# Kernel tuning notes

Measured on AMD Instinct MI355X. Metric: run time of the kernel, lower is better.

The kernel has to match this reference:

```python
import jax, jax.numpy as jnp
import numpy as np

HID = 128
GRID = 8
PRED_LEN = 25


def _lstm_final(x, w_ih, w_hh, b_ih, b_hh):
    """PyTorch-style LSTM over time axis; returns final (h, c). x: [B, T, F]."""
    B = x.shape[0]
    H = w_hh.shape[1]
    # precompute input contribution for all timesteps: [B, T, 4H]
    gx = jnp.einsum('btf,gf->btg', x, w_ih) + b_ih + b_hh

    def step(carry, g):
        h, c = carry
        gates = g + h @ w_hh.T
        i, f, gg, o = jnp.split(gates, 4, axis=-1)  # torch gate order i,f,g,o
        i = jax.nn.sigmoid(i)
        f = jax.nn.sigmoid(f)
        gg = jnp.tanh(gg)
        o = jax.nn.sigmoid(o)
        c = f * c + i * gg
        h = o * jnp.tanh(c)
        return (h, c), None

    h0 = jnp.zeros((B, H), x.dtype)
    (h, c), _ = jax.lax.scan(step, (h0, h0), jnp.swapaxes(gx, 0, 1))
    return h, c


def _conv2d_same(x, w, b):
    y = jax.lax.conv_general_dilated(x, w, (1, 1), 'SAME',
                                     dimension_numbers=('NCHW', 'OIHW', 'NCHW'))
    return y + b[None, :, None, None]


def setup_inputs() -> dict:
    key = jax.random.key(0)
    ks = jax.random.split(key, 24)
    B, K, T, F = 8192, 8, 20, 7
    H = HID
    s = lambda fan: 1.0 / np.sqrt(fan)
    u = lambda k, shape, fan: jax.random.uniform(k, shape, jnp.float32, -s(fan), s(fan))
    inp = {
        'target': jax.random.normal(ks[0], (B, T, F), jnp.float32),
        'neigh_dyn': jax.random.normal(ks[1], (B, K, T, F), jnp.float32),
        'neigh_spatial': jax.random.normal(ks[2], (B, K, 2), jnp.float32),
        'lane': jax.random.normal(ks[3], (B, T), jnp.float32),
        # encoder LSTM
        'enc_w_ih': u(ks[4], (4 * H, F), H), 'enc_w_hh': u(ks[5], (4 * H, H), H),
        'enc_b_ih': u(ks[6], (4 * H,), H), 'enc_b_hh': u(ks[7], (4 * H,), H),
        # neighbor encoder LSTM
        'nb_w_ih': u(ks[8], (4 * H, F), H), 'nb_w_hh': u(ks[9], (4 * H, H), H),
        'nb_b_ih': u(ks[10], (4 * H,), H), 'nb_b_hh': u(ks[11], (4 * H,), H),
        # social conv stack
        'conv1_w': u(ks[12], (H // 2, H, 3, 3), H * 9), 'conv1_b': u(ks[13], (H // 2,), H * 9),
        'conv2_w': u(ks[14], (H // 4, H // 2, 3, 3), (H // 2) * 9), 'conv2_b': u(ks[15], (H // 4,), (H // 2) * 9),
        # fusion linear (H + H//4 -> H)
        'fus_w': u(ks[16], (H, H + H // 4), H + H // 4), 'fus_b': u(ks[17], (H,), H + H // 4),
        # decoder LSTM (input_dim 2)
        'dec_w_ih': u(ks[18], (4 * H, 2), H), 'dec_w_hh': u(ks[19], (4 * H, H), H),
        'dec_b_ih': u(ks[20], (4 * H,), H), 'dec_b_hh': u(ks[21], (4 * H,), H),
        # output linear (H -> 2)
        'out_w': u(ks[22], (2, H), H), 'out_b': u(ks[23], (2,), H),
    }
    return inp


def reference(target, neigh_dyn, neigh_spatial, lane,
              enc_w_ih, enc_w_hh, enc_b_ih, enc_b_hh,
              nb_w_ih, nb_w_hh, nb_b_ih, nb_b_hh,
              conv1_w, conv1_b, conv2_w, conv2_b,
              fus_w, fus_b,
              dec_w_ih, dec_w_hh, dec_b_ih, dec_b_hh,
              out_w, out_b):
    B = target.shape[0]
    K = neigh_dyn.shape[1]
    H = HID

    # encode target trajectory
    h_target, _ = _lstm_final(target, enc_w_ih, enc_w_hh, enc_b_ih, enc_b_hh)  # [B, H]

    # encode neighbors (shared weights) via flattening B*K
    neigh_flat = neigh_dyn.reshape(B * K, neigh_dyn.shape[2], neigh_dyn.shape[3])
    h_neigh, _ = _lstm_final(neigh_flat, nb_w_ih, nb_w_hh, nb_b_ih, nb_b_hh)
    h_neigh = h_neigh.reshape(B, K, H)

    # social pooling: scatter into [B, H, GRID, GRID]
    center = GRID // 2
    n = min(K, GRID * GRID - 1)
    idx = np.arange(n) + 1
    xs = idx % GRID
    ys = idx // GRID
    grid = jnp.zeros((B, H, GRID, GRID), target.dtype)
    grid = grid.at[:, :, center, center].set(h_target)
    grid = grid.at[:, :, ys, xs].set(jnp.swapaxes(h_neigh[:, :n, :], 1, 2))

    x = jax.nn.relu(_conv2d_same(grid, conv1_w, conv1_b))
    x = jax.nn.relu(_conv2d_same(x, conv2_w, conv2_b))
    pooled = jnp.max(x, axis=(2, 3))  # AdaptiveMaxPool2d(1) -> [B, H//4]

    fused = jnp.tanh(jnp.concatenate([h_target, pooled], axis=-1) @ fus_w.T + fus_b)

    dec_bias = dec_b_ih + dec_b_hh

    def dec_step(carry, _):
        h, c, inp = carry
        gates = inp @ dec_w_ih.T + h @ dec_w_hh.T + dec_bias
        i, f, gg, o = jnp.split(gates, 4, axis=-1)
        i = jax.nn.sigmoid(i)
        f = jax.nn.sigmoid(f)
        gg = jnp.tanh(gg)
        o = jax.nn.sigmoid(o)
        c = f * c + i * gg
        h = o * jnp.tanh(c)
        pred = h @ out_w.T + out_b  # [B, 2]
        return (h, c, pred), pred

    h0 = fused
    c0 = jnp.zeros_like(fused)
    inp0 = jnp.zeros((B, 2), target.dtype)
    _, preds = jax.lax.scan(dec_step, (h0, c0, inp0), None, length=PRED_LEN)
    return jnp.swapaxes(preds, 0, 1)  # [B, pred_len, 2]
```

## Files before the change

kernel.cpp:

```cpp
#include <hip/hip_runtime.h>

typedef _Float16 half8  __attribute__((ext_vector_type(8)));
typedef _Float16 half4v __attribute__((ext_vector_type(4)));
typedef float  floatx4  __attribute__((ext_vector_type(4)));

#define MFMA16(A,B,C) __builtin_amdgcn_mfma_f32_16x16x32_f16((A),(B),(C),0,0,0)

#define L2E  1.4426950408889634f
#define L2E2 2.8853900817779268f

__device__ __forceinline__ float rcpf(float x){ return __builtin_amdgcn_rcpf(x); }
__device__ __forceinline__ float ex2(float x){ return __builtin_amdgcn_exp2f(x); }
__device__ __forceinline__ float tanh_raw(float c){
  return 1.0f - 2.0f*rcpf(1.0f + ex2(L2E2*c));
}
__device__ __forceinline__ half8 ld8(const _Float16* p){
  half4v a = *(const half4v*)p;
  half4v b = *(const half4v*)(p+4);
  return __builtin_shufflevector(a,b,0,1,2,3,4,5,6,7);
}

__device__ __forceinline__ float lstm_cell(float yi, float yf, float yg, float yo,
                                           float& c){
  float A = ex2(-yi), B = ex2(-yf), C = ex2(yg);
  float r1 = rcpf(1.0f + B);
  float r2 = rcpf((1.0f + A)*(1.0f + C));
  float cn = c*r1 + (C - 1.0f)*r2;
  c = cn;
  float F = ex2(-yo), E = ex2(L2E2*cn);
  float r3 = rcpf((1.0f + F)*(1.0f + E));
  return (E - 1.0f)*r3;
}

static __device__ constexpr int DY[27] = {0,0,0,0,0,0,0,0, 1,1,1,1,1,1,1,1, 2,2, 3,3,3,4,4,4,5,5,5};
static __device__ constexpr int DX[27] = {0,1,2,3,4,5,6,7, 0,1,2,3,4,5,6,7, 0,1, 3,4,5,3,4,5,3,4,5};
static __device__ constexpr int PY[9]  = {0,0,0,0,0,0,0,1,4};
static __device__ constexpr int PX[9]  = {1,2,3,4,5,6,7,0,4};
static __device__ constexpr int OY[46] = {0,0,0,0,0,0,0,0, 1,1,1,1,1,1,1,1, 2,2,2,2,2,2,2,2,
                                          3,3,3,3,3,3,3, 4,4,4,4,4, 5,5,5,5,5, 6,6,6,6,6};
static __device__ constexpr int OX[46] = {0,1,2,3,4,5,6,7, 0,1,2,3,4,5,6,7, 0,1,2,3,4,5,6,7,
                                          0,1,2,3,4,5,6, 2,3,4,5,6, 2,3,4,5,6, 2,3,4,5,6};
__device__ constexpr int d1idx(int iy,int ix){
  return (iy<0||iy>7||ix<0||ix>7) ? -1 :
         (iy<=1) ? iy*8+ix :
         (iy==2 && ix<=1) ? 16+ix :
         (iy>=3 && iy<=5 && ix>=3 && ix<=5) ? 18+(iy-3)*3+(ix-3) : -1;
}

__global__ __launch_bounds__(512, 4) void lstm_all(
    const float* __restrict__ target, const float* __restrict__ neigh,
    const float* __restrict__ e_wih, const float* __restrict__ e_whh,
    const float* __restrict__ e_bih, const float* __restrict__ e_bhh,
    const float* __restrict__ n_wih, const float* __restrict__ n_whh,
    const float* __restrict__ n_bih, const float* __restrict__ n_bhh,
    _Float16* __restrict__ h_enc16, _Float16* __restrict__ h_nb16)
{
  __shared__ _Float16 h_lds[2][16][136];
  __shared__ _Float16 xf16[16][168];
  __shared__ __align__(16) _Float16 wihb[8][4][17][8];

  const int tid  = threadIdx.x;
  const int wv   = tid >> 6;
  const int lane = tid & 63;
  const int q    = lane >> 4;
  const int cb   = lane & 15;

  const bool enc = (blockIdx.x < 512);
  const float* x   = enc ? target : neigh;
  const float* wih = enc ? e_wih : n_wih;
  const float* whh = enc ? e_whh : n_whh;
  const float* bih = enc ? e_bih : n_bih;
  const float* bhh = enc ? e_bhh : n_bhh;
  _Float16* hout   = enc ? h_enc16 : h_nb16;
  const long base  = enc ? (long)blockIdx.x*16 : (long)(blockIdx.x-512)*16;

  for (int i = tid; i < 16*168; i += 512){
    int seq = i/168, rem = i%168, t = rem>>3, f = rem&7;
    float v = 0.f;
    if (t < 20) v = (f < 7) ? x[base*140 + seq*140 + t*7 + f] : 1.0f;
    xf16[seq][rem] = (_Float16)v;
  }
  for (int i = tid; i < 2*16*136; i += 512) ((_Float16*)h_lds)[i] = (_Float16)0.f;

  if (q == 0){
    #pragma unroll
    for (int g=0; g<4; ++g){
      const float sc = (g==2) ? L2E2 : L2E;
      const int col = g*128 + wv*16 + cb;
      _Float16* d = &wihb[wv][g][cb][0];
      #pragma unroll
      for (int j=0;j<7;++j) d[j] = (_Float16)(wih[col*7+j]*sc);
      d[7] = (_Float16)((bih[col]+bhh[col])*sc);
    }
  } else if (lane == 16){
    #pragma unroll
    for (int g=0; g<4; ++g){
      _Float16* d = &wihb[wv][g][16][0];
      #pragma unroll
      for (int j=0;j<8;++j) d[j] = (_Float16)0.f;
    }
  }

  half8 bfrag[4][4];
  #pragma unroll
  for (int g=0; g<4; ++g){
    const float sc = (g==2) ? L2E2 : L2E;
    const int col = g*128 + wv*16 + cb;
    #pragma unroll
    for (int kc=0; kc<4; ++kc){
      const float* src = whh + (long)col*128 + kc*32 + q*8;
      half8 f;
      #pragma unroll
      for (int j=0;j<8;++j) f[j] = (_Float16)(src[j]*sc);
      bfrag[g][kc] = f;
    }
  }
  __syncthreads();

  const _Float16* bxp = &wihb[wv][0][(q==0)?cb:16][0];
  const _Float16* a4p = (q==0) ? &xf16[cb][0] : &wihb[wv][0][16][0];
  const int a4step = (q==0) ? 8 : 0;
  half8 a4 = *(const half8*)a4p;
  a4p += a4step;

  float c_reg[4] = {0,0,0,0};
  half4v hv = {0,0,0,0};
  const floatx4 ZERO4 = {0.f,0.f,0.f,0.f};

  for (int t=0; t<20; ++t){
    const _Float16* hrow = &h_lds[t&1][cb][0];

    floatx4 acc[4];
    #pragma unroll
    for (int g=0; g<4; ++g){
      half8 bx = *(const half8*)(bxp + g*136);
      acc[g] = MFMA16(bx, a4, ZERO4);
    }
    #pragma unroll
    for (int kc=0; kc<4; ++kc){
      half8 b = *(const half8*)(hrow + kc*32 + q*8);
      #pragma unroll
      for (int g=0; g<4; ++g)
        acc[g] = MFMA16(bfrag[g][kc], b, acc[g]);
    }
    #pragma unroll
    for (int r=0; r<4; ++r)
      hv[r] = (_Float16)lstm_cell(acc[0][r], acc[1][r], acc[2][r], acc[3][r], c_reg[r]);
    *(half4v*)&h_lds[(t+1)&1][cb][wv*16 + q*4] = hv;
    a4 = *(const half8*)a4p;
    a4p += a4step;
    __syncthreads();
  }

  *(half4v*)&hout[(base + cb)*128 + wv*16 + q*4] = hv;
}

__global__ void prep_kernel(const float* __restrict__ w1, const float* __restrict__ b1,
                            const float* __restrict__ w2, const float* __restrict__ b2,
                            const float* __restrict__ fus_w,
                            const float* __restrict__ dec_wih, const float* __restrict__ dec_whh,
                            const float* __restrict__ dec_bih, const float* __restrict__ dec_bhh,
                            const float* __restrict__ out_w, const float* __restrict__ out_b,
                            _Float16* __restrict__ w1f, _Float16* __restrict__ w2f,
                            _Float16* __restrict__ fus_wf,
                            _Float16* __restrict__ whhp, float* __restrict__ biasp,
                            float* __restrict__ v2bg, float* __restrict__ bgmax)
{
  const int tid = threadIdx.x;
  const int gid = blockIdx.x*256 + tid;
  const int gstride = gridDim.x*256;
  for (int i = gid; i < 9*64*128; i += gstride){
    int s = i>>13, rem = i&8191, c1 = rem>>7, ci = rem&127;
    w1f[s*8448 + c1*132 + ci] = (_Float16)w1[c1*1152 + ci*9 + s];
  }
  for (int i = gid; i < 9*32*64; i += gstride){
    int s = i>>11, rem = i&2047, c2 = rem>>6, ci = rem&63;
    w2f[s*2176 + c2*68 + ci] = (_Float16)w2[c2*576 + ci*9 + s];
  }
  for (int i = gid; i < 128*160; i += gstride){
    int n = i/160, k = i%160;
    fus_wf[n*164 + k] = (_Float16)fus_w[i];
  }
  for (int i = gid; i < 512*128; i += gstride){
    int col = i>>7, k = i&127;
    float sc = ((col>>7)==2) ? L2E2 : L2E;
    float v = dec_whh[i] + dec_wih[col*2+0]*out_w[k] + dec_wih[col*2+1]*out_w[128+k];
    whhp[i] = (_Float16)(v*sc);
  }
  for (int i = gid; i < 512; i += gstride){
    float sc = ((i>>7)==2) ? L2E2 : L2E;
    biasp[i] = (dec_bih[i] + dec_bhh[i] + dec_wih[i*2+0]*out_b[0]
                + dec_wih[i*2+1]*out_b[1])*sc;
  }
  if (blockIdx.x == 0){
    __shared__ float S[288];
    __shared__ int bgm[32];
    for (int i=tid;i<288;i+=256){
      int c2=i/9, s=i%9;
      float a=0.f;
      for (int ci=0;ci<64;++ci) a += w2[c2*576+ci*9+s]*fmaxf(b1[ci],0.f);
      S[i]=a;
    }
    if (tid<32) bgm[tid]=0;
    __syncthreads();
    for (int i=tid;i<2048;i+=256){
      int cell=i>>5, c2=i&31, y=cell>>3, xx=cell&7;
      float a=b2[c2];
      for (int dy=0;dy<3;++dy){ int iy=y+dy-1; if((unsigned)iy>7u) continue;
        for (int dx=0;dx<3;++dx){ int ix=xx+dx-1; if((unsigned)ix>7u) continue;
          a += S[c2*9+dy*3+dx]; } }
      v2bg[cell*32+c2]=a;
      bool aff = (y<=2) || (y==3 && xx<=6) || (y>=4 && y<=6 && xx>=2 && xx<=6);
      if(!aff) atomicMax(&bgm[c2], __float_as_int(fmaxf(a,0.f)));
    }
    __syncthreads();
    if (tid<32) bgmax[tid]=__int_as_float(bgm[tid]);
  }
}

__global__ __launch_bounds__(512, 1) void social_fuse(
    const _Float16* __restrict__ h_enc, const _Float16* __restrict__ h_nb,
    const _Float16* __restrict__ w1f, const _Float16* __restrict__ w2f,
    const _Float16* __restrict__ fus_wf,
    const float* __restrict__ b1, const float* __restrict__ v2bg,
    const float* __restrict__ bgmax, const float* __restrict__ fus_b,
    float* __restrict__ fused)
{
  __shared__ __align__(16) _Float16 vecs[9*16*132];
  __shared__ __align__(16) _Float16 d1[27*16*68];
  __shared__ __align__(16) _Float16 A16[16*164];
  __shared__ int pooled[512];

  const int tid  = threadIdx.x;
  const int wv   = tid >> 6;
  const int lane = tid & 63;
  const int q    = lane >> 4;
  const int cb   = lane & 15;
  const long base = (long)blockIdx.x * 16;

  for (int i=tid; i<9*16*32; i+=512){
    int p = i>>9, rem = i&511, bb = rem>>5, j = rem&31;
    const _Float16* src = (p<8) ? (h_nb + (((base+bb))*8 + p)*128 + j*4)
                                : (h_enc + (base+bb)*128 + j*4);
    *(unsigned long long*)(vecs + p*2112 + bb*132 + j*4) = *(const unsigned long long*)src;
  }
  for (int i=tid; i<512; i+=512){
    int bb=i>>5, j=i&31;
    *(unsigned long long*)(A16 + bb*164 + j*4) =
        *(const unsigned long long*)(h_enc + (base+bb)*128 + j*4);
  }
  for (int i=tid; i<512; i+=512) pooled[i] = __float_as_int(bgmax[i&31]);
  __syncthreads();

  {
    const int c1lane = (wv&3)*16 + cb;
    const int half   = wv >> 2;
    half8 bf1[9][4];
    #pragma unroll
    for (int s=0;s<9;++s)
      #pragma unroll
      for (int kc=0;kc<4;++kc)
        bf1[s][kc] = ld8(w1f + s*8448 + c1lane*132 + kc*32 + q*8);
    const float b1v = b1[c1lane];
    const float bg  = fmaxf(b1v, 0.f);

    #pragma unroll
    for (int ci=0; ci<27; ++ci){
      if ((ci & 1) != half) continue;
      const int y = DY[ci], x = DX[ci];
      floatx4 C = {0.f,0.f,0.f,0.f};
      #pragma unroll
      for (int p=0;p<9;++p){
        const int dy = PY[p]-y+1, dx = PX[p]-x+1;
        if (dy>=0 && dy<3 && dx>=0 && dx<3){
          const int s = dy*3+dx;
          const _Float16* ap = vecs + p*2112 + cb*132 + q*8;
          #pragma unroll
          for (int kc=0;kc<4;++kc)
            C = MFMA16(ld8(ap + kc*32), bf1[s][kc], C);
        }
      }
      _Float16* dp = d1 + ci*1088 + c1lane;
      #pragma unroll
      for (int r=0;r<4;++r)
        dp[(q*4+r)*68] = (_Float16)(fmaxf(b1v + C[r], 0.f) - bg);
    }
  }
  __syncthreads();

  {
    half8 bf2[9][2][2];
    #pragma unroll
    for (int s=0;s<9;++s)
      #pragma unroll
      for (int nt=0;nt<2;++nt)
        #pragma unroll
        for (int kc=0;kc<2;++kc)
          bf2[s][nt][kc] = ld8(w2f + s*2176 + (nt*16+cb)*68 + kc*32 + q*8);

    float rm0[4] = {0,0,0,0}, rm1[4] = {0,0,0,0};
    #pragma unroll
    for (int oc=0; oc<46; ++oc){
      if ((oc & 7) != wv) continue;
      const int y = OY[oc], x = OX[oc];
      const int cell = y*8+x;
      float v0 = v2bg[cell*32 + cb];
      float v1 = v2bg[cell*32 + 16 + cb];
      floatx4 C0 = {v0,v0,v0,v0}, C1 = {v1,v1,v1,v1};
      #pragma unroll
      for (int dy=0;dy<3;++dy)
        #pragma unroll
        for (int dx=0;dx<3;++dx){
          const int dc = d1idx(y+dy-1, x+dx-1);
          if (dc < 0) continue;
          const int s = dy*3+dx;
          const _Float16* ap = d1 + dc*1088 + cb*68 + q*8;
          #pragma unroll
          for (int kc=0;kc<2;++kc){
            half8 a = ld8(ap + kc*32);
            C0 = MFMA16(a, bf2[s][0][kc], C0);
            C1 = MFMA16(a, bf2[s][1][kc], C1);
          }
        }
      #pragma unroll
      for (int r=0;r<4;++r){
        rm0[r] = fmaxf(rm0[r], fmaxf(C0[r],0.f));
        rm1[r] = fmaxf(rm1[r], fmaxf(C1[r],0.f));
      }
    }
    #pragma unroll
    for (int r=0;r<4;++r){
      atomicMax(&pooled[(q*4+r)*32 + cb],      __float_as_int(rm0[r]));
      atomicMax(&pooled[(q*4+r)*32 + 16 + cb], __float_as_int(rm1[r]));
    }
  }
  __syncthreads();

  for (int i=tid;i<512;i+=512){
    int bb=i>>5, c2=i&31;
    A16[bb*164 + 128 + c2] = (_Float16)__int_as_float(pooled[i]);
  }
  __syncthreads();

  {
    half8 bfF[5];
    #pragma unroll
    for (int kc=0;kc<5;++kc)
      bfF[kc] = ld8(fus_wf + (wv*16+cb)*164 + kc*32 + q*8);
    const float fb = fus_b[wv*16+cb];
    floatx4 C0 = {0.f,0.f,0.f,0.f};
    #pragma unroll
    for (int kc=0;kc<5;++kc){
      half8 a = ld8(A16 + cb*164 + kc*32 + q*8);
      C0 = MFMA16(a, bfF[kc], C0);
    }
    #pragma unroll
    for (int r=0;r<4;++r){
      const long row = base + q*4 + r;
      fused[row*128 + wv*16+cb] = tanh_raw(C0[r]+fb);
    }
  }
}

__global__ __launch_bounds__(512, 4) void dec_mfma(
    const float* __restrict__ fused,
    const _Float16* __restrict__ whhp, const float* __restrict__ biasp,
    const float* __restrict__ w_ih,
    const float* __restrict__ out_w, const float* __restrict__ out_b,
    float* __restrict__ out)
{
  __shared__ _Float16 h_lds[2][16][136];
  __shared__ __align__(16) _Float16 wib[8][4][17][8];
  __shared__ float ow_lds[2][128];
  __shared__ float pred_lds[16][2];

  const int tid  = threadIdx.x;
  const int wv   = tid >> 6;
  const int lane = tid & 63;
  const int q    = lane >> 4;
  const int cb   = lane & 15;
  const long base = (long)blockIdx.x * 16;

  for (int i=tid;i<256;i+=512) ow_lds[i>>7][i&127] = out_w[i];
  for (int i=tid;i<2048;i+=512) h_lds[0][i>>7][i&127] = (_Float16)fused[base*128 + i];
  for (int i=tid;i<2048;i+=512) h_lds[1][i>>7][i&127] = (_Float16)0.f;

  if (q == 0){
    #pragma unroll
    for (int g=0; g<4; ++g){
      const float sc = (g==2) ? L2E2 : L2E;
      const int col = g*128 + wv*16 + cb;
      _Float16* d = &wib[wv][g][cb][0];
      d[0] = (_Float16)(-w_ih[col*2+0]*sc);
      d[1] = (_Float16)(-w_ih[col*2+1]*sc);
      #pragma unroll
      for (int j=2;j<8;++j) d[j] = (_Float16)0.f;
    }
  } else if (lane == 16){
    #pragma unroll
    for (int g=0; g<4; ++g){
      _Float16* d = &wib[wv][g][16][0];
      #pragma unroll
      for (int j=0;j<8;++j) d[j] = (_Float16)0.f;
    }
  }

  half8 bfrag[4][4];
  float bias_r[4][4];
  #pragma unroll
  for (int g=0; g<4; ++g){
    const int col = g*128 + wv*16 + cb;
    #pragma unroll
    for (int r=0; r<4; ++r) bias_r[g][r] = biasp[g*128 + wv*16 + q*4 + r];
    #pragma unroll
    for (int kc=0; kc<4; ++kc)
      bfrag[g][kc] = ld8(whhp + (long)col*128 + kc*32 + q*8);
  }
  float ob0 = out_b[0], ob1 = out_b[1];
  __syncthreads();

  {
    int pair = tid>>3, part = tid&7;
    if (pair < 32){
      int m = pair>>1, oc = pair&1;
      const float* owp = ow_lds[oc];
      float v = 0.f;
      #pragma unroll
      for (int k=part*16; k<part*16+16; ++k) v += owp[k]*(float)h_lds[0][m][k];
      v += __shfl_down(v, 4, 8);
      v += __shfl_down(v, 2, 8);
      v += __shfl_down(v, 1, 8);
      if (part==0) pred_lds[m][oc] = v + (oc ? ob1 : ob0);
    }
  }
  __syncthreads();

  const _Float16* wibp = &wib[wv][0][(q==0)?cb:16][0];
  float c_reg[4] = {0,0,0,0};
  half4v hv;

  for (int t=0; t<25; ++t){
    const _Float16* hrow = &h_lds[t&1][cb][0];

    floatx4 acc[4];
    #pragma unroll
    for (int g=0; g<4; ++g)
      #pragma unroll
      for (int r=0; r<4; ++r) acc[g][r] = bias_r[g][r];

    if (t == 0){
      half8 pb = {0,0,0,0,0,0,0,0};
      if (q == 0){
        pb[0] = (_Float16)pred_lds[cb][0];
        pb[1] = (_Float16)pred_lds[cb][1];
      }
      #pragma unroll
      for (int g=0; g<4; ++g){
        half8 w = *(const half8*)(wibp + g*136);
        acc[g] = MFMA16(w, pb, acc[g]);
      }
    }
    #pragma unroll
    for (int kc=0; kc<4; ++kc){
      half8 b = *(const half8*)(hrow + kc*32 + q*8);
      #pragma unroll
      for (int g=0; g<4; ++g)
        acc[g] = MFMA16(bfrag[g][kc], b, acc[g]);
    }
    #pragma unroll
    for (int r=0; r<4; ++r)
      hv[r] = (_Float16)lstm_cell(acc[0][r], acc[1][r], acc[2][r], acc[3][r], c_reg[r]);
    _Float16 (*hw)[136] = h_lds[(t+1)&1];
    *(half4v*)&hw[cb][wv*16 + q*4] = hv;
    __syncthreads();
    {
      int pair = tid>>3, part = tid&7;
      if (pair < 32){
        int m = pair>>1, oc = pair&1;
        const float* owp = ow_lds[oc];
        float v = 0.f;
        #pragma unroll
        for (int k=part*16; k<part*16+16; ++k) v += owp[k]*(float)hw[m][k];
        v += __shfl_down(v, 4, 8);
        v += __shfl_down(v, 2, 8);
        v += __shfl_down(v, 1, 8);
        if (part==0)
          out[(base+m)*50 + t*2 + oc] = v + (oc ? ob1 : ob0);
      }
    }
  }
}

extern "C" void kernel_launch(void* const* d_in, const int* in_sizes, int n_in,
                              void* d_out, int out_size, void* d_ws, size_t ws_size,
                              hipStream_t stream)
{
  (void)in_sizes; (void)n_in; (void)out_size; (void)ws_size;
  const float* target   = (const float*)d_in[0];
  const float* neigh    = (const float*)d_in[1];
  const float* enc_w_ih = (const float*)d_in[4];
  const float* enc_w_hh = (const float*)d_in[5];
  const float* enc_b_ih = (const float*)d_in[6];
  const float* enc_b_hh = (const float*)d_in[7];
  const float* nb_w_ih  = (const float*)d_in[8];
  const float* nb_w_hh  = (const float*)d_in[9];
  const float* nb_b_ih  = (const float*)d_in[10];
  const float* nb_b_hh  = (const float*)d_in[11];
  const float* w1       = (const float*)d_in[12];
  const float* b1       = (const float*)d_in[13];
  const float* w2       = (const float*)d_in[14];
  const float* b2       = (const float*)d_in[15];
  const float* fus_w    = (const float*)d_in[16];
  const float* fus_b    = (const float*)d_in[17];
  const float* dec_w_ih = (const float*)d_in[18];
  const float* dec_w_hh = (const float*)d_in[19];
  const float* dec_b_ih = (const float*)d_in[20];
  const float* dec_b_hh = (const float*)d_in[21];
  const float* out_w    = (const float*)d_in[22];
  const float* out_b    = (const float*)d_in[23];

  char* ws = (char*)d_ws;
  _Float16* h_nb16  = (_Float16*)ws;
  _Float16* h_enc16 = (_Float16*)(ws + (16u<<20));
  float*    fusedp  = (float*)(ws + (18u<<20));
  char* aux = ws + (22u<<20);
  _Float16* w1f    = (_Float16*)aux;
  _Float16* w2f    = (_Float16*)(aux + 152064);
  _Float16* fus_wf = (_Float16*)(aux + 152064 + 39168);
  float*    v2bg   = (float*)(aux + 233216);
  float*    bgmaxp = (float*)(aux + 241408);
  _Float16* whhp   = (_Float16*)(aux + 241536);
  float*    biasp  = (float*)(aux + 241536 + 131072);

  prep_kernel<<<64, 256, 0, stream>>>(w1, b1, w2, b2, fus_w,
                                      dec_w_ih, dec_w_hh, dec_b_ih, dec_b_hh,
                                      out_w, out_b,
                                      w1f, w2f, fus_wf, whhp, biasp, v2bg, bgmaxp);
  lstm_all<<<4608, 512, 0, stream>>>(target, neigh,
                                     enc_w_ih, enc_w_hh, enc_b_ih, enc_b_hh,
                                     nb_w_ih, nb_w_hh, nb_b_ih, nb_b_hh,
                                     h_enc16, h_nb16);
  social_fuse<<<512, 512, 0, stream>>>(h_enc16, h_nb16, w1f, w2f, fus_wf,
                                       b1, v2bg, bgmaxp, fus_b, fusedp);
  dec_mfma<<<512, 512, 0, stream>>>(fusedp, whhp, biasp, dec_w_ih,
                                    out_w, out_b, (float*)d_out);
}
```

Before: 494.5 us.

## Process two 16-sequence tiles per LSTM block to reuse recurrent weights

The encoder/neighbor LSTM kernel now handles 32 sequences per block as two interleaved 16-row MFMA tiles, halving the grid. The per-block setup cost (loading and converting W_hh into register fragments, building W_ih tiles) is spread over twice as many sequences, and two independent recurrence chains per wave give the scheduler more latency to hide. Separately, the LSTM cell math merges two reciprocals into one using a common denominator. This adds LDS and register pressure, and the fused reciprocal could lose precision or overflow at extreme gate values.

```diff
diff --git a/kernel.cpp b/kernel.cpp
--- a/kernel.cpp
+++ b/kernel.cpp
@@ -23,9 +23,10 @@
 __device__ __forceinline__ float lstm_cell(float yi, float yf, float yg, float yo,
                                            float& c){
   float A = ex2(-yi), B = ex2(-yf), C = ex2(yg);
-  float r1 = rcpf(1.0f + B);
-  float r2 = rcpf((1.0f + A)*(1.0f + C));
-  float cn = c*r1 + (C - 1.0f)*r2;
+  float P = (1.0f + A)*(1.0f + C);
+  float Q = 1.0f + B;
+  float r = rcpf(P*Q);
+  float cn = (c*P + (C - 1.0f)*Q)*r;
   c = cn;
   float F = ex2(-yo), E = ex2(L2E2*cn);
   float r3 = rcpf((1.0f + F)*(1.0f + E));
@@ -55,8 +56,8 @@
     const float* __restrict__ n_bih, const float* __restrict__ n_bhh,
     _Float16* __restrict__ h_enc16, _Float16* __restrict__ h_nb16)
 {
-  __shared__ _Float16 h_lds[2][16][136];
-  __shared__ _Float16 xf16[16][168];
+  __shared__ _Float16 h_lds[2][32][136];
+  __shared__ _Float16 xf16[32][168];
   __shared__ __align__(16) _Float16 wihb[8][4][17][8];
 
   const int tid  = threadIdx.x;
@@ -65,22 +66,22 @@
   const int q    = lane >> 4;
   const int cb   = lane & 15;
 
-  const bool enc = (blockIdx.x < 512);
+  const bool enc = (blockIdx.x < 256);
   const float* x   = enc ? target : neigh;
   const float* wih = enc ? e_wih : n_wih;
   const float* whh = enc ? e_whh : n_whh;
   const float* bih = enc ? e_bih : n_bih;
   const float* bhh = enc ? e_bhh : n_bhh;
   _Float16* hout   = enc ? h_enc16 : h_nb16;
-  const long base  = enc ? (long)blockIdx.x*16 : (long)(blockIdx.x-512)*16;
-
-  for (int i = tid; i < 16*168; i += 512){
+  const long base  = enc ? (long)blockIdx.x*32 : (long)(blockIdx.x-256)*32;
+
+  for (int i = tid; i < 32*168; i += 512){
     int seq = i/168, rem = i%168, t = rem>>3, f = rem&7;
     float v = 0.f;
     if (t < 20) v = (f < 7) ? x[base*140 + seq*140 + t*7 + f] : 1.0f;
     xf16[seq][rem] = (_Float16)v;
   }
-  for (int i = tid; i < 2*16*136; i += 512) ((_Float16*)h_lds)[i] = (_Float16)0.f;
+  for (int i = tid; i < 2*32*136; i += 512) ((_Float16*)h_lds)[i] = (_Float16)0.f;
 
   if (q == 0){
     #pragma unroll
@@ -118,41 +119,65 @@
   __syncthreads();
 
   const _Float16* bxp = &wihb[wv][0][(q==0)?cb:16][0];
-  const _Float16* a4p = (q==0) ? &xf16[cb][0] : &wihb[wv][0][16][0];
-  const int a4step = (q==0) ? 8 : 0;
-  half8 a4 = *(const half8*)a4p;
-  a4p += a4step;
-
-  float c_reg[4] = {0,0,0,0};
-  half4v hv = {0,0,0,0};
+  const _Float16* zsrc = &wihb[wv][0][16][0];
+  const _Float16* a0p = (q==0) ? &xf16[cb][0]    : zsrc;
+  const _Float16* a1p = (q==0) ? &xf16[cb+16][0] : zsrc;
+  const int astep = (q==0) ? 8 : 0;
+  half8 a40 = *(const half8*)a0p; a0p += astep;
+  half8 a41 = *(const half8*)a1p; a1p += astep;
+
+  float c0[4] = {0,0,0,0}, c1[4] = {0,0,0,0};
+  half4v hv0 = {0,0,0,0}, hv1 = {0,0,0,0};
   const floatx4 ZERO4 = {0.f,0.f,0.f,0.f};
 
   for (int t=0; t<20; ++t){
-    const _Float16* hrow = &h_lds[t&1][cb][0];
-
-    floatx4 acc[4];
-    #pragma unroll
-    for (int g=0; g<4; ++g){
-      half8 bx = *(const half8*)(bxp + g*136);
-      acc[g] = MFMA16(bx, a4, ZERO4);
-    }
-    #pragma unroll
-    for (int kc=0; kc<4; ++kc){
-      half8 b = *(const half8*)(hrow + kc*32 + q*8);
-      #pragma unroll
-      for (int g=0; g<4; ++g)
-        acc[g] = MFMA16(bfrag[g][kc], b, acc[g]);
-    }
-    #pragma unroll
-    for (int r=0; r<4; ++r)
-      hv[r] = (_Float16)lstm_cell(acc[0][r], acc[1][r], acc[2][r], acc[3][r], c_reg[r]);
-    *(half4v*)&h_lds[(t+1)&1][cb][wv*16 + q*4] = hv;
-    a4 = *(const half8*)a4p;
-    a4p += a4step;
+    {
+      const _Float16* hrow = &h_lds[t&1][cb][0];
+      floatx4 acc[4];
+      #pragma unroll
+      for (int g=0; g<4; ++g){
+        half8 bx = *(const half8*)(bxp + g*136);
+        acc[g] = MFMA16(bx, a40, ZERO4);
+      }
+      #pragma unroll
+      for (int kc=0; kc<4; ++kc){
+        half8 b = *(const half8*)(hrow + kc*32 + q*8);
+        #pragma unroll
+        for (int g=0; g<4; ++g)
+          acc[g] = MFMA16(bfrag[g][kc], b, acc[g]);
+      }
+      #pragma unroll
+      for (int r=0; r<4; ++r)
+        hv0[r] = (_Float16)lstm_cell(acc[0][r], acc[1][r], acc[2][r], acc[3][r], c0[r]);
+      *(half4v*)&h_lds[(t+1)&1][cb][wv*16 + q*4] = hv0;
+    }
+    {
+      const _Float16* hrow = &h_lds[t&1][cb+16][0];
+      floatx4 acc[4];
+      #pragma unroll
+      for (int g=0; g<4; ++g){
+        half8 bx = *(const half8*)(bxp + g*136);
+        acc[g] = MFMA16(bx, a41, ZERO4);
+      }
+      #pragma unroll
+      for (int kc=0; kc<4; ++kc){
+        half8 b = *(const half8*)(hrow + kc*32 + q*8);
+        #pragma unroll
+        for (int g=0; g<4; ++g)
+          acc[g] = MFMA16(bfrag[g][kc], b, acc[g]);
+      }
+      #pragma unroll
+      for (int r=0; r<4; ++r)
+        hv1[r] = (_Float16)lstm_cell(acc[0][r], acc[1][r], acc[2][r], acc[3][r], c1[r]);
+      *(half4v*)&h_lds[(t+1)&1][cb+16][wv*16 + q*4] = hv1;
+    }
+    a40 = *(const half8*)a0p; a0p += astep;
+    a41 = *(const half8*)a1p; a1p += astep;
     __syncthreads();
   }
 
-  *(half4v*)&hout[(base + cb)*128 + wv*16 + q*4] = hv;
+  *(half4v*)&hout[(base + cb)*128      + wv*16 + q*4] = hv0;
+  *(half4v*)&hout[(base + cb + 16)*128 + wv*16 + q*4] = hv1;
 }
 
 __global__ void prep_kernel(const float* __restrict__ w1, const float* __restrict__ b1,
@@ -536,7 +561,7 @@
                                       dec_w_ih, dec_w_hh, dec_b_ih, dec_b_hh,
                                       out_w, out_b,
                                       w1f, w2f, fus_wf, whhp, biasp, v2bg, bgmaxp);
-  lstm_all<<<4608, 512, 0, stream>>>(target, neigh,
+  lstm_all<<<2304, 512, 0, stream>>>(target, neigh,
                                      enc_w_ih, enc_w_hh, enc_b_ih, enc_b_hh,
                                      nb_w_ih, nb_w_hh, nb_b_ih, nb_b_hh,
                                      h_enc16, h_nb16);
```

After: 497.9 us. Within noise of the previous version (+0.7%).
